# Performance work log

Hardware: AMD Instinct MI355X
Metric: run time of the kernel (lower is better)

The kernel has to match this reference:

```python
import jax, jax.numpy as jnp
import numpy as np

N_NODES = 50000


def gcn_conv(x, W, b, row, col, num_nodes):
    """PyG-style GCNConv: out = D^{-1/2}(A+I)D^{-1/2} (x @ W) + b.

    row/col already include self-loops. x: [N, Fin], W: [Fin, Fout].
    """
    h = x @ W  # [N, Fout]
    deg = jax.ops.segment_sum(jnp.ones_like(col, dtype=h.dtype), col,
                              num_segments=num_nodes)  # in-degree incl. self-loop
    dinv = jnp.where(deg > 0, jax.lax.rsqrt(deg), 0.0)
    norm = dinv[row] * dinv[col]  # [E]
    msgs = h[row] * norm[:, None]  # gather + scale, [E, Fout]
    out = jax.ops.segment_sum(msgs, col, num_segments=num_nodes)  # scatter-add
    return out + b


def setup_inputs() -> dict:
    key = jax.random.key(0)
    k1, k2, k3, k4 = jax.random.split(key, 4)
    Fin, Fh, Fout = 128, 128, 64
    E = 800000
    x = jax.random.normal(k1, (N_NODES, Fin), dtype=jnp.float32)
    edge_index = jax.random.randint(k2, (2, E), 0, N_NODES, dtype=jnp.int64)
    # Glorot-ish init for weights
    W1 = jax.random.normal(k3, (Fin, Fh), dtype=jnp.float32) / np.sqrt(Fin)
    b1 = jnp.zeros((Fh,), dtype=jnp.float32)
    W2 = jax.random.normal(k4, (Fh, Fout), dtype=jnp.float32) / np.sqrt(Fh)
    b2 = jnp.zeros((Fout,), dtype=jnp.float32)
    return {"x": x, "edge_index": edge_index, "W1": W1, "b1": b1,
            "W2": W2, "b2": b2}


def reference(x, edge_index, W1, b1, W2, b2):
    n = x.shape[0]
    # add self-loops once (shared by both conv layers)
    loops = jnp.arange(n, dtype=edge_index.dtype)
    row = jnp.concatenate([edge_index[0], loops])
    col = jnp.concatenate([edge_index[1], loops])
    h = jax.nn.relu(gcn_conv(x, W1, b1, row, col, n))
    # dropout(p=0.5) is identity in eval mode (self.training == False)
    return gcn_conv(h, W2, b2, row, col, n)
```

## Files before the change

### kernel.cpp

```cpp
#include <hip/hip_runtime.h>


constexpr int KD = 128;
constexpr int CHUNK = 4096;
constexpr int BCAP = 6144;

using short8  = __attribute__((ext_vector_type(8))) short;
using float4v = __attribute__((ext_vector_type(4))) float;


__device__ __forceinline__ unsigned short f2bf(float f) {
    unsigned int u = __float_as_uint(f);
    u = (u + 0x7fffu + ((u >> 16) & 1u)) >> 16;
    return (unsigned short)u;
}

__device__ __forceinline__ float2 bfpair(unsigned int u) {
    float2 f;
    f.x = __uint_as_float(u << 16);
    f.y = __uint_as_float(u & 0xffff0000u);
    return f;
}

__device__ __forceinline__ unsigned int packbf(float x, float y) {
    return (unsigned int)f2bf(x) | ((unsigned int)f2bf(y) << 16);
}

__device__ __forceinline__ void bfsplit(float x, unsigned short& h, unsigned short& l) {
    h = f2bf(x);
    float fh = __uint_as_float((unsigned int)h << 16);
    l = f2bf(x - fh);
}

__global__ __launch_bounds__(128) void setup(const float* __restrict__ W1,
                                             unsigned short* __restrict__ Wth1,
                                             unsigned short* __restrict__ Wtl1,
                                             const float* __restrict__ W2,
                                             unsigned short* __restrict__ Wth2,
                                             unsigned short* __restrict__ Wtl2,
                                             int* __restrict__ gcur) {
    int b = blockIdx.x;
    int n = threadIdx.x;
    int k = b & 127;
    if (b == 0) {
        gcur[n] = n * BCAP;
        gcur[n + 128] = (n + 128) * BCAP;
    }
    if (b < 128) {
        float w = W1[k * 128 + n];
        unsigned short h, l;
        bfsplit(w, h, l);
        Wth1[n * KD + k] = h;
        Wtl1[n * KD + k] = l;
    } else if (n < 64) {
        float w = W2[k * 64 + n];
        unsigned short h, l;
        bfsplit(w, h, l);
        Wth2[n * KD + k] = h;
        Wtl2[n * KD + k] = l;
    }
}


__global__ __launch_bounds__(256) void bucket_scatter(const int* __restrict__ row,
                                                      const int* __restrict__ col,
                                                      int* gcur,
                                                      unsigned int* __restrict__ bpack,
                                                      int E) {
    __shared__ int lh[256];
    __shared__ int lbase[256];
    lh[threadIdx.x] = 0;
    __syncthreads();
    int base = blockIdx.x * CHUNK;
#pragma unroll
    for (int r = 0; r < CHUNK / 256; ++r) {
        int e = base + r * 256 + threadIdx.x;
        if (e < E) atomicAdd(&lh[col[e] >> 8], 1);
    }
    __syncthreads();
    int c0 = lh[threadIdx.x];
    lbase[threadIdx.x] = c0 ? atomicAdd(&gcur[threadIdx.x], c0) : 0;
    __syncthreads();
    lh[threadIdx.x] = 0;
    __syncthreads();
#pragma unroll
    for (int r = 0; r < CHUNK / 256; ++r) {
        int e = base + r * 256 + threadIdx.x;
        if (e < E) {
            int c = col[e];
            int b = c >> 8;
            int slot = lbase[b] + atomicAdd(&lh[b], 1);
            bpack[slot] = ((unsigned int)row[e] << 16) | (unsigned int)c;
        }
    }
}

__global__ __launch_bounds__(256) void bucket_csr(const unsigned int* __restrict__ bpack,
                                                  const int* __restrict__ gcur,
                                                  int* __restrict__ rowptr,
                                                  float* __restrict__ dinv,
                                                  unsigned short* __restrict__ srow,
                                                  int N, int E) {
    __shared__ int s[256];
    __shared__ int lh[256];
    __shared__ int lcur[256];
    __shared__ int sh_bstart;
    int b = blockIdx.x;
    int t = threadIdx.x;
    int cntb = gcur[t] - t * BCAP;
    s[t] = cntb;
    __syncthreads();
    for (int off = 1; off < 256; off <<= 1) {
        int tv = (t >= off) ? s[t - off] : 0;
        __syncthreads();
        s[t] += tv;
        __syncthreads();
    }
    if (t == b) sh_bstart = s[t] - cntb;
    if (b == 0 && t == 0) rowptr[N] = E;
    lh[t] = 0;
    __syncthreads();
    int bstart = sh_bstart;
    int nE = gcur[b] - b * BCAP;
    int base = b * BCAP;
    for (int i = t; i < nE; i += 256)
        atomicAdd(&lh[bpack[base + i] & 255], 1);
    __syncthreads();
    int v = lh[t];
    s[t] = v;
    __syncthreads();
    for (int off = 1; off < 256; off <<= 1) {
        int tv = (t >= off) ? s[t - off] : 0;
        __syncthreads();
        s[t] += tv;
        __syncthreads();
    }
    int myStart = bstart + s[t] - v;
    int node = (b << 8) + t;
    if (node < N) {
        rowptr[node] = myStart;
        dinv[node] = rsqrtf(1.0f + (float)v);
    }
    lcur[t] = myStart;
    __syncthreads();
    for (int i = t; i < nE; i += 256) {
        unsigned int p = bpack[base + i];
        int slot = atomicAdd(&lcur[p & 255], 1);
        srow[slot] = (unsigned short)(p >> 16);
    }
}

__global__ __launch_bounds__(256) void gemm_mfma1(const float* __restrict__ X,
                                                  const unsigned short* __restrict__ Wth,
                                                  const unsigned short* __restrict__ Wtl,
                                                  const float* __restrict__ dinv,
                                                  unsigned short* __restrict__ G, int N) {
    constexpr int FOUT = 128, NT = 8;
    int wave = threadIdx.x >> 6;
    int lane = threadIdx.x & 63;
    int row0 = (blockIdx.x * 4 + wave) * 16;
    if (row0 >= N) return;
    int m = lane & 15;
    int quad = lane >> 4;

    float4v acc[NT];
#pragma unroll
    for (int ct = 0; ct < NT; ++ct) acc[ct] = (float4v){0.f, 0.f, 0.f, 0.f};

    const float* xrow = X + (size_t)(row0 + m) * KD + quad * 8;

#pragma unroll
    for (int ks = 0; ks < 4; ++ks) {
        float4 xa = *(const float4*)(xrow + ks * 32);
        float4 xb = *(const float4*)(xrow + ks * 32 + 4);
        float xs[8] = {xa.x, xa.y, xa.z, xa.w, xb.x, xb.y, xb.z, xb.w};
        short8 ah, al;
#pragma unroll
        for (int j = 0; j < 8; ++j) {
            unsigned short h, l;
            bfsplit(xs[j], h, l);
            ah[j] = (short)h;
            al[j] = (short)l;
        }
        int koff = ks * 32 + quad * 8;
#pragma unroll
        for (int ct = 0; ct < NT; ++ct) {
            const unsigned short* wb = Wth + (size_t)(ct * 16 + m) * KD + koff;
            const unsigned short* wl = Wtl + (size_t)(ct * 16 + m) * KD + koff;
            short8 bh = *(const short8*)wb;
            short8 bl = *(const short8*)wl;
            acc[ct] = __builtin_amdgcn_mfma_f32_16x16x32_bf16(ah, bh, acc[ct], 0, 0, 0);
            acc[ct] = __builtin_amdgcn_mfma_f32_16x16x32_bf16(al, bh, acc[ct], 0, 0, 0);
            acc[ct] = __builtin_amdgcn_mfma_f32_16x16x32_bf16(ah, bl, acc[ct], 0, 0, 0);
        }
    }

#pragma unroll
    for (int r = 0; r < 4; ++r) {
        int row = row0 + quad * 4 + r;
        float s = dinv[row];
#pragma unroll
        for (int ct = 0; ct < NT; ++ct) {
            G[(size_t)row * FOUT + ct * 16 + m] = f2bf(acc[ct][r] * s);
        }
    }
}

__global__ __launch_bounds__(256) void gemm_mfma2(const unsigned short* __restrict__ H,
                                                  const unsigned short* __restrict__ Wth,
                                                  const unsigned short* __restrict__ Wtl,
                                                  const float* __restrict__ dinv,
                                                  unsigned short* __restrict__ G, int N) {
    constexpr int FOUT = 64, NT = 4;
    int wave = threadIdx.x >> 6;
    int lane = threadIdx.x & 63;
    int row0 = (blockIdx.x * 4 + wave) * 16;
    if (row0 >= N) return;
    int m = lane & 15;
    int quad = lane >> 4;

    float4v acc[NT];
#pragma unroll
    for (int ct = 0; ct < NT; ++ct) acc[ct] = (float4v){0.f, 0.f, 0.f, 0.f};

    const unsigned short* hrow = H + (size_t)(row0 + m) * KD + quad * 8;

#pragma unroll
    for (int ks = 0; ks < 4; ++ks) {
        short8 a = *(const short8*)(hrow + ks * 32);
        int koff = ks * 32 + quad * 8;
#pragma unroll
        for (int ct = 0; ct < NT; ++ct) {
            short8 bh = *(const short8*)(Wth + (size_t)(ct * 16 + m) * KD + koff);
            short8 bl = *(const short8*)(Wtl + (size_t)(ct * 16 + m) * KD + koff);
            acc[ct] = __builtin_amdgcn_mfma_f32_16x16x32_bf16(a, bh, acc[ct], 0, 0, 0);
            acc[ct] = __builtin_amdgcn_mfma_f32_16x16x32_bf16(a, bl, acc[ct], 0, 0, 0);
        }
    }

#pragma unroll
    for (int r = 0; r < 4; ++r) {
        int row = row0 + quad * 4 + r;
        float s = dinv[row];
#pragma unroll
        for (int ct = 0; ct < 4; ++ct) {
            G[(size_t)row * FOUT + ct * 16 + m] = f2bf(acc[ct][r] * s);
        }
    }
}

template <bool RELU>
__global__ __launch_bounds__(256) void gather128(const int* __restrict__ rowptr,
                                                 const unsigned short* __restrict__ srow,
                                                 const unsigned int* __restrict__ G,
                                                 const float* __restrict__ dinv,
                                                 const float* __restrict__ bias,
                                                 unsigned int* __restrict__ H2,
                                                 int N) {
    int node = (blockIdx.x * 256 + threadIdx.x) >> 6;
    int lane = threadIdx.x & 63;
    if (node >= N) return;
    int beg = rowptr[node];
    int end = rowptr[node + 1];

    float ax, ay;
    {
        float2 s0 = bfpair(G[(size_t)node * 64 + lane]);
        ax = s0.x; ay = s0.y;
    }

    for (int e = beg; e < end; e += 8) {
        unsigned int u[8];
#pragma unroll
        for (int j = 0; j < 8; ++j) {
            int idx = e + j;
            idx = (idx < end) ? idx : (end - 1);
            int r = __builtin_amdgcn_readfirstlane((int)srow[idx]);
            const unsigned int* p = G + (size_t)r * 64;
            u[j] = p[lane];
        }
        float sx = 0.f, sy = 0.f;
#pragma unroll
        for (int j = 0; j < 8; ++j) {
            unsigned int uv = (e + j < end) ? u[j] : 0u;
            float2 v = bfpair(uv);
            sx += v.x; sy += v.y;
        }
        ax += sx; ay += sy;
    }
    float s = dinv[node];
    float2 bv = ((const float2*)bias)[lane];
    float ox = ax * s + bv.x;
    float oy = ay * s + bv.y;
    if (RELU) { ox = fmaxf(ox, 0.f); oy = fmaxf(oy, 0.f); }
    __builtin_nontemporal_store(packbf(ox, oy), &H2[(size_t)node * 64 + lane]);
}

template <bool RELU>
__global__ __launch_bounds__(256) void gather64(const int* __restrict__ rowptr,
                                                const unsigned short* __restrict__ srow,
                                                const unsigned int* __restrict__ G,
                                                const float* __restrict__ dinv,
                                                const float* __restrict__ bias,
                                                float* __restrict__ O, int N) {
    int tid = blockIdx.x * 256 + threadIdx.x;
    int node = tid >> 5;
    int lane = threadIdx.x & 31;
    if (node >= N) return;
    int beg = rowptr[node];
    int end = rowptr[node + 1];

    float2 s0 = bfpair(G[(size_t)node * 32 + lane]);
    float ax = s0.x, ay = s0.y;

    for (int e = beg; e < end; e += 8) {
        unsigned int u[8];
#pragma unroll
        for (int j = 0; j < 8; ++j) {
            int idx = e + j;
            idx = (idx < end) ? idx : (end - 1);
            int r = (int)srow[idx];
            u[j] = G[(size_t)r * 32 + lane];
        }
        float sx = 0.f, sy = 0.f;
#pragma unroll
        for (int j = 0; j < 8; ++j) {
            unsigned int uv = (e + j < end) ? u[j] : 0u;
            float2 v = bfpair(uv);
            sx += v.x; sy += v.y;
        }
        ax += sx; ay += sy;
    }
    float s = dinv[node];
    float2 bv = ((const float2*)bias)[lane];
    float ox = ax * s + bv.x;
    float oy = ay * s + bv.y;
    if (RELU) { ox = fmaxf(ox, 0.f); oy = fmaxf(oy, 0.f); }
    float2 o = make_float2(ox, oy);
    unsigned long long p;
    __builtin_memcpy(&p, &o, 8);
    __builtin_nontemporal_store(p, (unsigned long long*)&((float2*)O)[(size_t)node * 32 + lane]);
}

extern "C" void kernel_launch(void* const* d_in, const int* in_sizes, int n_in,
                              void* d_out, int out_size, void* d_ws, size_t ws_size,
                              hipStream_t stream) {
    const float* x  = (const float*)d_in[0];
    const int*   ei = (const int*)d_in[1];
    const float* W1 = (const float*)d_in[2];
    const float* b1 = (const float*)d_in[3];
    const float* W2 = (const float*)d_in[4];
    const float* b2 = (const float*)d_in[5];
    float* out = (float*)d_out;

    int N = in_sizes[0] / 128;
    int E = in_sizes[1] / 2;
    const int* row = ei;
    const int* col = ei + E;

    char* ws = (char*)d_ws;
    float* dinv   = (float*)(ws + 0x000000);
    int*   rowptr = (int*)  (ws + 0x080000);
    int*   gcur   = (int*)  (ws + 0x0F9000);
    unsigned short* srow = (unsigned short*)(ws + 0x100000);
    unsigned short* g1 = (unsigned short*)(ws + 0x440000);
    unsigned short* wth1 = (unsigned short*)(ws + 0x10C0000);
    unsigned short* wtl1 = (unsigned short*)(ws + 0x10D0000);
    unsigned short* wth2 = (unsigned short*)(ws + 0x10E0000);
    unsigned short* wtl2 = (unsigned short*)(ws + 0x10F0000);
    unsigned short* h2 = (unsigned short*)(ws + 0x1200000);
    unsigned short* g2 = (unsigned short*)(ws + 0x2C00000);
    unsigned int* bpack = (unsigned int*)(ws + 0x1200000);

    int NB_BKT  = (E + CHUNK - 1) / CHUNK;
    int NBUCKET = (N + 255) / 256;

    setup<<<256, 128, 0, stream>>>(W1, wth1, wtl1, W2, wth2, wtl2, gcur);
    bucket_scatter<<<NB_BKT, 256, 0, stream>>>(row, col, gcur, bpack, E);
    bucket_csr<<<NBUCKET, 256, 0, stream>>>(bpack, gcur, rowptr, dinv, srow, N, E);

    int nb;
    nb = (N + 63) / 64;
    gemm_mfma1<<<nb, 256, 0, stream>>>(x, wth1, wtl1, dinv, g1, N);
    nb = (N + 3) / 4;
    gather128<true><<<nb, 256, 0, stream>>>(rowptr, srow, (const unsigned int*)g1,
                                            dinv, b1, (unsigned int*)h2, N);

    nb = (N + 63) / 64;
    gemm_mfma2<<<nb, 256, 0, stream>>>(h2, wth2, wtl2, dinv, g2, N);
    nb = (N + 7) / 8;
    gather64<false><<<nb, 256, 0, stream>>>(rowptr, srow, (const unsigned int*)g2,
                                            dinv, b2, out, N);
}
```

Baseline: 210.2 us.

## Fuse CSR build with first GEMM and move source normalization into gather

Merges the bucket CSR kernel and the first-layer MFMA GEMM into one launch, split by block index, so the GEMM runs alongside CSR construction. The GEMM no longer depends on dinv, so the source-side dinv scaling moves into gather128, which now loads dinv per neighbor and uses an FMA. The bucket scatter chunk size is also halved to create more blocks. This removes a launch and lets two independent stages overlap, at the cost of extra per-edge dinv loads in the layer-1 gather.

```diff
diff --git a/kernel.cpp b/kernel.cpp
--- a/kernel.cpp
+++ b/kernel.cpp
@@ -2,7 +2,7 @@
 
 
 constexpr int KD = 128;
-constexpr int CHUNK = 4096;
+constexpr int CHUNK = 2048;
 constexpr int BCAP = 6144;
 
 using short8  = __attribute__((ext_vector_type(8))) short;
@@ -61,7 +61,6 @@
     }
 }
 
-
 __global__ __launch_bounds__(256) void bucket_scatter(const int* __restrict__ row,
                                                       const int* __restrict__ col,
                                                       int* gcur,
@@ -95,113 +94,109 @@
     }
 }
 
-__global__ __launch_bounds__(256) void bucket_csr(const unsigned int* __restrict__ bpack,
-                                                  const int* __restrict__ gcur,
-                                                  int* __restrict__ rowptr,
-                                                  float* __restrict__ dinv,
-                                                  unsigned short* __restrict__ srow,
-                                                  int N, int E) {
+__global__ __launch_bounds__(256) void csr_and_gemm1(
+        const unsigned int* __restrict__ bpack, const int* __restrict__ gcur,
+        int* __restrict__ rowptr, float* __restrict__ dinv,
+        unsigned short* __restrict__ srow, int N, int E, int NBUCKET,
+        const float* __restrict__ X,
+        const unsigned short* __restrict__ Wth,
+        const unsigned short* __restrict__ Wtl,
+        unsigned short* __restrict__ G) {
     __shared__ int s[256];
     __shared__ int lh[256];
     __shared__ int lcur[256];
     __shared__ int sh_bstart;
-    int b = blockIdx.x;
-    int t = threadIdx.x;
-    int cntb = gcur[t] - t * BCAP;
-    s[t] = cntb;
-    __syncthreads();
-    for (int off = 1; off < 256; off <<= 1) {
-        int tv = (t >= off) ? s[t - off] : 0;
-        __syncthreads();
-        s[t] += tv;
-        __syncthreads();
-    }
-    if (t == b) sh_bstart = s[t] - cntb;
-    if (b == 0 && t == 0) rowptr[N] = E;
-    lh[t] = 0;
-    __syncthreads();
-    int bstart = sh_bstart;
-    int nE = gcur[b] - b * BCAP;
-    int base = b * BCAP;
-    for (int i = t; i < nE; i += 256)
-        atomicAdd(&lh[bpack[base + i] & 255], 1);
-    __syncthreads();
-    int v = lh[t];
-    s[t] = v;
-    __syncthreads();
-    for (int off = 1; off < 256; off <<= 1) {
-        int tv = (t >= off) ? s[t - off] : 0;
-        __syncthreads();
-        s[t] += tv;
-        __syncthreads();
-    }
-    int myStart = bstart + s[t] - v;
-    int node = (b << 8) + t;
-    if (node < N) {
-        rowptr[node] = myStart;
-        dinv[node] = rsqrtf(1.0f + (float)v);
-    }
-    lcur[t] = myStart;
-    __syncthreads();
-    for (int i = t; i < nE; i += 256) {
-        unsigned int p = bpack[base + i];
-        int slot = atomicAdd(&lcur[p & 255], 1);
-        srow[slot] = (unsigned short)(p >> 16);
-    }
-}
-
-__global__ __launch_bounds__(256) void gemm_mfma1(const float* __restrict__ X,
-                                                  const unsigned short* __restrict__ Wth,
-                                                  const unsigned short* __restrict__ Wtl,
-                                                  const float* __restrict__ dinv,
-                                                  unsigned short* __restrict__ G, int N) {
-    constexpr int FOUT = 128, NT = 8;
-    int wave = threadIdx.x >> 6;
-    int lane = threadIdx.x & 63;
-    int row0 = (blockIdx.x * 4 + wave) * 16;
-    if (row0 >= N) return;
-    int m = lane & 15;
-    int quad = lane >> 4;
-
-    float4v acc[NT];
-#pragma unroll
-    for (int ct = 0; ct < NT; ++ct) acc[ct] = (float4v){0.f, 0.f, 0.f, 0.f};
-
-    const float* xrow = X + (size_t)(row0 + m) * KD + quad * 8;
-
-#pragma unroll
-    for (int ks = 0; ks < 4; ++ks) {
-        float4 xa = *(const float4*)(xrow + ks * 32);
-        float4 xb = *(const float4*)(xrow + ks * 32 + 4);
-        float xs[8] = {xa.x, xa.y, xa.z, xa.w, xb.x, xb.y, xb.z, xb.w};
-        short8 ah, al;
-#pragma unroll
-        for (int j = 0; j < 8; ++j) {
-            unsigned short h, l;
-            bfsplit(xs[j], h, l);
-            ah[j] = (short)h;
-            al[j] = (short)l;
-        }
-        int koff = ks * 32 + quad * 8;
-#pragma unroll
-        for (int ct = 0; ct < NT; ++ct) {
-            const unsigned short* wb = Wth + (size_t)(ct * 16 + m) * KD + koff;
-            const unsigned short* wl = Wtl + (size_t)(ct * 16 + m) * KD + koff;
-            short8 bh = *(const short8*)wb;
-            short8 bl = *(const short8*)wl;
-            acc[ct] = __builtin_amdgcn_mfma_f32_16x16x32_bf16(ah, bh, acc[ct], 0, 0, 0);
-            acc[ct] = __builtin_amdgcn_mfma_f32_16x16x32_bf16(al, bh, acc[ct], 0, 0, 0);
-            acc[ct] = __builtin_amdgcn_mfma_f32_16x16x32_bf16(ah, bl, acc[ct], 0, 0, 0);
-        }
-    }
-
-#pragma unroll
-    for (int r = 0; r < 4; ++r) {
-        int row = row0 + quad * 4 + r;
-        float s = dinv[row];
-#pragma unroll
-        for (int ct = 0; ct < NT; ++ct) {
-            G[(size_t)row * FOUT + ct * 16 + m] = f2bf(acc[ct][r] * s);
+
+    if ((int)blockIdx.x < NBUCKET) {
+        int b = blockIdx.x;
+        int t = threadIdx.x;
+        int cntb = gcur[t] - t * BCAP;
+        s[t] = cntb;
+        __syncthreads();
+        for (int off = 1; off < 256; off <<= 1) {
+            int tv = (t >= off) ? s[t - off] : 0;
+            __syncthreads();
+            s[t] += tv;
+            __syncthreads();
+        }
+        if (t == b) sh_bstart = s[t] - cntb;
+        if (b == 0 && t == 0) rowptr[N] = E;
+        lh[t] = 0;
+        __syncthreads();
+        int bstart = sh_bstart;
+        int nE = gcur[b] - b * BCAP;
+        int base = b * BCAP;
+        for (int i = t; i < nE; i += 256)
+            atomicAdd(&lh[bpack[base + i] & 255], 1);
+        __syncthreads();
+        int v = lh[t];
+        s[t] = v;
+        __syncthreads();
+        for (int off = 1; off < 256; off <<= 1) {
+            int tv = (t >= off) ? s[t - off] : 0;
+            __syncthreads();
+            s[t] += tv;
+            __syncthreads();
+        }
+        int myStart = bstart + s[t] - v;
+        int node = (b << 8) + t;
+        if (node < N) {
+            rowptr[node] = myStart;
+            dinv[node] = rsqrtf(1.0f + (float)v);
+        }
+        lcur[t] = myStart;
+        __syncthreads();
+        for (int i = t; i < nE; i += 256) {
+            unsigned int p = bpack[base + i];
+            int slot = atomicAdd(&lcur[p & 255], 1);
+            srow[slot] = (unsigned short)(p >> 16);
+        }
+    } else {
+        constexpr int FOUT = 128, NT = 8;
+        int wave = threadIdx.x >> 6;
+        int lane = threadIdx.x & 63;
+        int row0 = (((int)blockIdx.x - NBUCKET) * 4 + wave) * 16;
+        if (row0 >= N) return;
+        int m = lane & 15;
+        int quad = lane >> 4;
+
+        float4v acc[NT];
+#pragma unroll
+        for (int ct = 0; ct < NT; ++ct) acc[ct] = (float4v){0.f, 0.f, 0.f, 0.f};
+
+        const float* xrow = X + (size_t)(row0 + m) * KD + quad * 8;
+
+#pragma unroll
+        for (int ks = 0; ks < 4; ++ks) {
+            float4 xa = *(const float4*)(xrow + ks * 32);
+            float4 xb = *(const float4*)(xrow + ks * 32 + 4);
+            float xs[8] = {xa.x, xa.y, xa.z, xa.w, xb.x, xb.y, xb.z, xb.w};
+            short8 ah, al;
+#pragma unroll
+            for (int j = 0; j < 8; ++j) {
+                unsigned short h, l;
+                bfsplit(xs[j], h, l);
+                ah[j] = (short)h;
+                al[j] = (short)l;
+            }
+            int koff = ks * 32 + quad * 8;
+#pragma unroll
+            for (int ct = 0; ct < NT; ++ct) {
+                short8 bh = *(const short8*)(Wth + (size_t)(ct * 16 + m) * KD + koff);
+                short8 bl = *(const short8*)(Wtl + (size_t)(ct * 16 + m) * KD + koff);
+                acc[ct] = __builtin_amdgcn_mfma_f32_16x16x32_bf16(ah, bh, acc[ct], 0, 0, 0);
+                acc[ct] = __builtin_amdgcn_mfma_f32_16x16x32_bf16(al, bh, acc[ct], 0, 0, 0);
+                acc[ct] = __builtin_amdgcn_mfma_f32_16x16x32_bf16(ah, bl, acc[ct], 0, 0, 0);
+            }
+        }
+
+#pragma unroll
+        for (int r = 0; r < 4; ++r) {
+            int row = row0 + quad * 4 + r;
+#pragma unroll
+            for (int ct = 0; ct < NT; ++ct) {
+                G[(size_t)row * FOUT + ct * 16 + m] = f2bf(acc[ct][r]);
+            }
         }
     }
 }
@@ -262,20 +257,23 @@
     if (node >= N) return;
     int beg = rowptr[node];
     int end = rowptr[node + 1];
+    float dn = dinv[node];
 
     float ax, ay;
     {
         float2 s0 = bfpair(G[(size_t)node * 64 + lane]);
-        ax = s0.x; ay = s0.y;
+        ax = s0.x * dn; ay = s0.y * dn;
     }
 
     for (int e = beg; e < end; e += 8) {
         unsigned int u[8];
+        float dr[8];
 #pragma unroll
         for (int j = 0; j < 8; ++j) {
             int idx = e + j;
             idx = (idx < end) ? idx : (end - 1);
             int r = __builtin_amdgcn_readfirstlane((int)srow[idx]);
+            dr[j] = dinv[r];
             const unsigned int* p = G + (size_t)r * 64;
             u[j] = p[lane];
         }
@@ -284,14 +282,14 @@
         for (int j = 0; j < 8; ++j) {
             unsigned int uv = (e + j < end) ? u[j] : 0u;
             float2 v = bfpair(uv);
-            sx += v.x; sy += v.y;
+            sx = fmaf(dr[j], v.x, sx);
+            sy = fmaf(dr[j], v.y, sy);
         }
         ax += sx; ay += sy;
     }
-    float s = dinv[node];
     float2 bv = ((const float2*)bias)[lane];
-    float ox = ax * s + bv.x;
-    float oy = ay * s + bv.y;
+    float ox = ax * dn + bv.x;
+    float oy = ay * dn + bv.y;
     if (RELU) { ox = fmaxf(ox, 0.f); oy = fmaxf(oy, 0.f); }
     __builtin_nontemporal_store(packbf(ox, oy), &H2[(size_t)node * 64 + lane]);
 }
@@ -374,14 +372,14 @@
 
     int NB_BKT  = (E + CHUNK - 1) / CHUNK;
     int NBUCKET = (N + 255) / 256;
+    int NB_GEMM1 = (N + 63) / 64;
 
     setup<<<256, 128, 0, stream>>>(W1, wth1, wtl1, W2, wth2, wtl2, gcur);
     bucket_scatter<<<NB_BKT, 256, 0, stream>>>(row, col, gcur, bpack, E);
-    bucket_csr<<<NBUCKET, 256, 0, stream>>>(bpack, gcur, rowptr, dinv, srow, N, E);
+    csr_and_gemm1<<<NBUCKET + NB_GEMM1, 256, 0, stream>>>(
+        bpack, gcur, rowptr, dinv, srow, N, E, NBUCKET, x, wth1, wtl1, g1);
 
     int nb;
-    nb = (N + 63) / 64;
-    gemm_mfma1<<<nb, 256, 0, stream>>>(x, wth1, wtl1, dinv, g1, N);
     nb = (N + 3) / 4;
     gather128<true><<<nb, 256, 0, stream>>>(rowptr, srow, (const unsigned int*)g1,
                                             dinv, b1, (unsigned int*)h2, N);
```

Result: faster. 196.2 us (-6.7%).
